# Performance work log

Hardware: AMD Instinct MI355X
Metric: run time of the kernel (lower is better)

Reference implementation:

```python
import jax, jax.numpy as jnp
import numpy as np

DIM, HEADS, DH, M, PINV_ITERS, RES_K = 512, 8, 64, 256, 6, 33

def layernorm(x, w, b, eps=1e-5):
    mu = jnp.mean(x, -1, keepdims=True)
    var = jnp.var(x, -1, keepdims=True)
    return (x - mu) * jax.lax.rsqrt(var + eps) * w + b

def pinv_iter(x, iters=PINV_ITERS):
    # Moore-Penrose iterative pseudo-inverse (lucidrains nystrom-attention)
    ax = jnp.abs(x)
    z = jnp.swapaxes(x, -1, -2) / (jnp.max(ax.sum(-1)) * jnp.max(ax.sum(-2)))
    I = jnp.eye(x.shape[-1], dtype=x.dtype)
    for _ in range(iters):
        xz = x @ z
        z = 0.25 * z @ (13 * I - xz @ (15 * I - xz @ (7 * I - xz)))
    return z

def _core(x, w_qkv):
    b, n, _ = x.shape
    pad = (M - n % M) % M            # Nystrom pads at the FRONT to a multiple of m=256
    xp = jnp.pad(x, ((0, 0), (pad, 0), (0, 0)))
    npad = n + pad
    q, k, v = jnp.split(xp @ w_qkv, 3, axis=-1)
    split_heads = lambda t: t.reshape(b, npad, HEADS, DH).transpose(0, 2, 1, 3)
    q = split_heads(q) * (DH ** -0.5)
    k, v = split_heads(k), split_heads(v)
    l = npad // M                    # tokens per landmark
    q_l = q.reshape(b, HEADS, M, l, DH).mean(3)
    k_l = k.reshape(b, HEADS, M, l, DH).mean(3)
    return q, k, v, q_l, k_l, pad, n

def nystrom_out(x, w_qkv, w_out, b_out, res_kernel):
    q, k, v, q_l, k_l, pad, n = _core(x, w_qkv)
    attn1 = jax.nn.softmax(jnp.einsum('bhid,bhjd->bhij', q, k_l), -1)    # (b,h,N,M)
    attn2 = jax.nn.softmax(jnp.einsum('bhid,bhjd->bhij', q_l, k_l), -1)  # (b,h,M,M)
    attn3 = jax.nn.softmax(jnp.einsum('bhid,bhjd->bhij', q_l, k), -1)    # (b,h,M,N)
    out = (attn1 @ pinv_iter(attn2)) @ (attn3 @ v)
    # depthwise residual conv over sequence dim, per head
    out = out + jax.lax.conv_general_dilated(
        v, res_kernel, (1, 1), [(RES_K // 2, RES_K // 2), (0, 0)],
        dimension_numbers=('NCHW', 'OIHW', 'NCHW'), feature_group_count=HEADS)
    b = out.shape[0]
    out = out.transpose(0, 2, 1, 3).reshape(b, -1, HEADS * DH) @ w_out + b_out
    return out[:, -n:]

def nystrom_cls_row(x, w_qkv):
    # cls-token (query index pad, head 0) row of attn1 @ pinv(attn2) @ attn3;
    # identical math to the full (n x n) matrix row the torch code slices out.
    q, k, v, q_l, k_l, pad, n = _core(x, w_qkv)
    q0, k0, ql0, kl0 = q[:, 0], k[:, 0], q_l[:, 0], k_l[:, 0]
    attn2 = jax.nn.softmax(ql0 @ jnp.swapaxes(kl0, -1, -2), -1)   # (b,M,M)
    attn3 = jax.nn.softmax(ql0 @ jnp.swapaxes(k0, -1, -2), -1)    # (b,M,N)
    row1 = jax.nn.softmax(jnp.einsum('bd,bjd->bj', q0[:, pad], kl0), -1)
    row = jnp.einsum('bj,bjk->bk', row1, pinv_iter(attn2))
    row = jnp.einsum('bk,bkn->bn', row, attn3)                    # (b, N_padded)
    return row, pad

def dwconv(x, k, b, p):
    y = jax.lax.conv_general_dilated(x, k, (1, 1), [(p, p), (p, p)],
        dimension_numbers=('NCHW', 'OIHW', 'NCHW'), feature_group_count=x.shape[1])
    return y + b[None, :, None, None]

def leff(x, k7, b7, k5, b5, k3, b3, Hs, Ws):
    cls_t, feat = x[:, :1], x[:, 1:]
    B, N, C = feat.shape
    img = feat.transpose(0, 2, 1).reshape(B, C, Hs, Ws)
    y = dwconv(img, k7, b7, 3) + img + dwconv(img, k5, b5, 2) + dwconv(img, k3, b3, 1)
    y = y.reshape(B, C, Hs * Ws).transpose(0, 2, 1)
    return jnp.concatenate([cls_t, y], axis=1)

def setup_inputs():
    key = jax.random.key(0)
    ks = iter(jax.random.split(key, 32))
    n, n_classes = 22500, 2
    p = {}
    p['h'] = jax.random.normal(next(ks), (n, 1024), jnp.float32)
    p['fc1_w'] = jax.random.normal(next(ks), (1024, DIM), jnp.float32) * 0.02
    p['fc1_b'] = jnp.zeros((DIM,), jnp.float32)
    p['cls_token'] = jax.random.normal(next(ks), (1, 1, DIM), jnp.float32)
    for pre in ('l1', 'l2'):
        p[pre + '_ln_w'] = jnp.ones((DIM,), jnp.float32)
        p[pre + '_ln_b'] = jnp.zeros((DIM,), jnp.float32)
        p[pre + '_wqkv'] = jax.random.normal(next(ks), (DIM, 3 * HEADS * DH), jnp.float32) * 0.02
        p[pre + '_wout'] = jax.random.normal(next(ks), (HEADS * DH, DIM), jnp.float32) * 0.02
        p[pre + '_bout'] = jnp.zeros((DIM,), jnp.float32)
        p[pre + '_resk'] = jax.random.normal(next(ks), (HEADS, 1, RES_K, 1), jnp.float32) * 0.05
    for kk in (7, 5, 3):
        p['leff_k%d' % kk] = jax.random.normal(next(ks), (DIM, 1, kk, kk), jnp.float32) * 0.05
        p['leff_b%d' % kk] = jnp.zeros((DIM,), jnp.float32)
    p['norm_w'] = jnp.ones((DIM,), jnp.float32)
    p['norm_b'] = jnp.zeros((DIM,), jnp.float32)
    p['fc2_w'] = jax.random.normal(next(ks), (DIM, n_classes), jnp.float32) * 0.02
    p['fc2_b'] = jnp.zeros((n_classes,), jnp.float32)
    return p

def reference(h, fc1_w, fc1_b, cls_token,
              l1_ln_w, l1_ln_b, l1_wqkv, l1_wout, l1_bout, l1_resk,
              leff_k7, leff_b7, leff_k5, leff_b5, leff_k3, leff_b3,
              l2_ln_w, l2_ln_b, l2_wqkv, l2_wout, l2_bout, l2_resk,
              norm_w, norm_b, fc2_w, fc2_b):
    x = h[None]                                   # (1, n, 1024)
    n = x.shape[1]
    x = jax.nn.relu(x @ fc1_w + fc1_b)            # (1, n, 512)
    Hs = int(np.ceil(np.sqrt(n)))                 # 150 for n=22500
    add_len = Hs * Hs - n
    if add_len > 0:
        x = jnp.concatenate([x, x[:, :add_len]], axis=1)
    x = jnp.concatenate([jnp.broadcast_to(cls_token, (1, 1, DIM)), x], axis=1)
    # TransLayer 1
    x = x + nystrom_out(layernorm(x, l1_ln_w, l1_ln_b), l1_wqkv, l1_wout, l1_bout, l1_resk)
    # LeFF positional layer
    x = leff(x, leff_k7, leff_b7, leff_k5, leff_b5, leff_k3, leff_b3, Hs, Hs)
    # TransLayer 2 (first call in TransMIL.forward)
    h2 = x + nystrom_out(layernorm(x, l2_ln_w, l2_ln_b), l2_wqkv, l2_wout, l2_bout, l2_resk)
    # TransLayer 2 second call: residual update then attention matrix of updated state
    h3 = h2 + nystrom_out(layernorm(h2, l2_ln_w, l2_ln_b), l2_wqkv, l2_wout, l2_bout, l2_resk)
    row, pad = nystrom_cls_row(layernorm(h3, l2_ln_w, l2_ln_b), l2_wqkv)
    A = row[0, pad + 1: pad + 1 + n][:, None]     # (n, 1) cls->instance attention
    hf = layernorm(h2, norm_w, norm_b)[:, 0]      # (1, 512)
    logits = hf @ fc2_w + fc2_b                   # (1, n_classes)
    Y_prob = jax.nn.softmax(logits, -1)
    return logits, Y_prob, A
```

## Files before the change

kernel.cpp:

```cpp
#include <hip/hip_runtime.h>

#define NTOK 22500
#define N1   22501
#define NPAD 22528
#define PADR 27
#define DIM  512
#define NH   8
#define DHD  64
#define MM   256
#define LLM  88
#define HSZ  150
#define CSZ  256
#define NCH  88

typedef short bf16x8 __attribute__((ext_vector_type(8)));
typedef float f32x4  __attribute__((ext_vector_type(4)));
typedef unsigned short us;

union U8 { bf16x8 v; unsigned short u[8]; };

__device__ __forceinline__ unsigned short f2b(float f){
  unsigned int u = __float_as_uint(f);
  unsigned int r = u + 0x7fffu + ((u>>16)&1u);
  return (unsigned short)(r>>16);
}
__device__ __forceinline__ float bf2f(unsigned short u){
  return __uint_as_float(((unsigned int)u)<<16);
}
__device__ __forceinline__ bf16x8 cvt8(float4 a, float4 b){
  U8 u;
  u.u[0]=f2b(a.x); u.u[1]=f2b(a.y); u.u[2]=f2b(a.z); u.u[3]=f2b(a.w);
  u.u[4]=f2b(b.x); u.u[5]=f2b(b.y); u.u[6]=f2b(b.z); u.u[7]=f2b(b.w);
  return u.v;
}
__device__ __forceinline__ void gld16(const void* g, void* l){
  __builtin_amdgcn_global_load_lds(
      (const __attribute__((address_space(1))) void*)g,
      (__attribute__((address_space(3))) void*)l, 16, 0, 0);
}

__device__ __forceinline__ float waveSum(float v){
#pragma unroll
  for (int o=32;o>0;o>>=1) v += __shfl_down(v,o);
  return v;
}
__device__ __forceinline__ float waveMax(float v){
#pragma unroll
  for (int o=32;o>0;o>>=1) v = fmaxf(v,__shfl_down(v,o));
  return v;
}
__device__ __forceinline__ float blockSum256(float v, float* sb){
  v = waveSum(v);
  __syncthreads();
  if ((threadIdx.x&63)==0) sb[threadIdx.x>>6]=v;
  __syncthreads();
  return sb[0]+sb[1]+sb[2]+sb[3];
}
__device__ __forceinline__ float blockMax256(float v, float* sb){
  v = waveMax(v);
  __syncthreads();
  if ((threadIdx.x&63)==0) sb[threadIdx.x>>6]=v;
  __syncthreads();
  return fmaxf(fmaxf(sb[0],sb[1]),fmaxf(sb[2],sb[3]));
}

__global__ void k_cvt(const float* __restrict__ src, us* __restrict__ dst, size_t n4)
{
  size_t i = ((size_t)blockIdx.x*256 + threadIdx.x);
  if (i < n4){
    float4 v = *(const float4*)(src + i*4);
    ushort4 u; u.x=f2b(v.x); u.y=f2b(v.y); u.z=f2b(v.z); u.w=f2b(v.w);
    *(ushort4*)(dst + i*4) = u;
  }
}

__global__ void k_wT(const float* __restrict__ W, us* __restrict__ Bt, int K, int N)
{
  __shared__ float tile[32][33];
  int tx = threadIdx.x&31, ty = threadIdx.x>>5;
  int k0 = blockIdx.x*32, n0 = blockIdx.y*32;
#pragma unroll
  for (int i=0;i<4;++i){
    int k = k0+ty+i*8;
    if (k<K && n0+tx<N) tile[ty+i*8][tx] = W[(size_t)k*N + n0+tx];
  }
  __syncthreads();
#pragma unroll
  for (int i=0;i<4;++i){
    int n = n0+ty+i*8, k = k0+tx;
    if (n<N && k<K) Bt[(size_t)n*K + k] = f2b(tile[tx][ty+i*8]);
  }
}

__global__ void k_vT(const us* __restrict__ V, us* __restrict__ Vt)
{
  __shared__ us tile[32][33];
  int tx = threadIdx.x&31, ty = threadIdx.x>>5;
  int p0 = blockIdx.x*32;
  int h = blockIdx.y>>1, d0 = (blockIdx.y&1)*32;
#pragma unroll
  for (int i=0;i<4;++i){
    int p = p0+ty+i*8;
    tile[ty+i*8][tx] = V[((size_t)h*NPAD+p)*DHD + d0+tx];
  }
  __syncthreads();
#pragma unroll
  for (int i=0;i<4;++i){
    int d = d0+ty+i*8;
    Vt[((size_t)h*DHD+d)*NPAD + p0+tx] = tile[tx][ty+i*8];
  }
}

template<int MODE>
__global__ __launch_bounds__(256) void k_gemm(
    const us* __restrict__ Ab, const us* __restrict__ Bt, const float* __restrict__ bias,
    us* __restrict__ Xb, float* __restrict__ Cf, float* __restrict__ C2,
    us* __restrict__ Q_, us* __restrict__ K_, us* __restrict__ V_,
    const us* __restrict__ zpg, int Kd, int mtn)
{
  constexpr int BM = 64;
  constexpr int BUFE = BM*64 + 128*64;
  __shared__ us SM[3*BUFE];
  const int tid = threadIdx.x;
  const int bid = blockIdx.x;
  const int ntile = bid / mtn;
  const int m0 = (bid % mtn)*BM, n0 = ntile*128;
  const int lane = tid & 63;
  const int wid = tid >> 6;
  const int wm = (wid>>1)*32, wn = (wid&1)*64;
  f32x4 acc[2][4] = {};
  const int NT = Kd >> 6;

  auto stage = [&](int t, int buf){
    us* As = SM + buf*BUFE;
    us* Bs = As + BM*64;
    int k0 = t*64;
#pragma unroll
    for (int i=0;i<2;++i){
      int c = wid*2+i;
      int row = c*8 + (lane>>3);
      int scol8 = ((lane&7) ^ (row&7))*8;
      int gm = m0+row;
      const us* ga;
      if (MODE==0)      ga = (gm<NTOK) ? Ab + (size_t)gm*Kd + k0 + scol8 : zpg + scol8;
      else if (MODE==2) ga = Ab + ((size_t)((gm<N1?gm:0)+PADR))*Kd + k0 + scol8;
      else              ga = (gm>=PADR) ? Ab + (size_t)(gm-PADR)*Kd + k0 + scol8 : zpg + scol8;
      gld16(ga, &As[c*512]);
    }
#pragma unroll
    for (int i=0;i<4;++i){
      int c = wid*4+i;
      int row = c*8 + (lane>>3);
      int scol8 = ((lane&7) ^ (row&7))*8;
      int vn = n0+row;
      if (MODE==3) vn = (vn<64)? vn : vn+448;
      gld16(Bt + (size_t)vn*Kd + k0 + scol8, &Bs[c*512]);
    }
  };

  stage(0, 0);
  stage(1, 1);
  for (int t=0; t<NT; ++t){
    asm volatile("s_waitcnt vmcnt(6)" ::: "memory");
    __builtin_amdgcn_s_barrier();
    asm volatile("" ::: "memory");
    if (t+2 < NT) stage(t+2, (t+2)%3);
    us* As = SM + (t%3)*BUFE;
    us* Bs = As + BM*64;
#pragma unroll
    for (int ks=0; ks<2; ++ks){
      const int kk = ks*32 + (lane>>4)*8;
      bf16x8 af[2], bfm[4];
#pragma unroll
      for (int tt=0;tt<2;++tt){
        int r = wm + tt*16 + (lane&15);
        af[tt] = *(bf16x8*)(&As[r*64 + (kk ^ ((r&7)<<3))]);
      }
#pragma unroll
      for (int tt=0;tt<4;++tt){
        int c = wn + tt*16 + (lane&15);
        bfm[tt] = *(bf16x8*)(&Bs[c*64 + (kk ^ ((c&7)<<3))]);
      }
#pragma unroll
      for (int mt=0;mt<2;++mt)
#pragma unroll
        for (int nt=0;nt<4;++nt)
          acc[mt][nt] = __builtin_amdgcn_mfma_f32_16x16x32_bf16(af[mt], bfm[nt], acc[mt][nt], 0,0,0);
    }
  }
  __syncthreads();
  const int rbase = (lane>>4)*4;
  const int cl = lane&15;
  if (MODE==3){
#pragma unroll
    for (int mt=0;mt<2;++mt)
#pragma unroll
      for (int r=0;r<4;++r){
        int gm = m0 + wm + mt*16 + rbase + r;
#pragma unroll
        for (int nt=0;nt<4;++nt){
          int gn = n0 + wn + nt*16 + cl;
          float v = acc[mt][nt][r];
          if (gn < 64) Cf[(size_t)gm*DHD + gn] = v*0.125f;
          else         C2[(size_t)gm*DHD + (gn-64)] = v;
        }
      }
    return;
  }
  const float sc1 = (MODE==1 && (ntile>>2)==0) ? 0.125f : 1.f;
#pragma unroll
  for (int mt=0;mt<2;++mt)
#pragma unroll
    for (int r=0;r<4;++r){
      int row = wm + mt*16 + rbase + r;
#pragma unroll
      for (int nt=0;nt<4;++nt){
        int col = wn + nt*16 + cl;
        float v = acc[mt][nt][r];
        if (MODE==0){ v += bias[n0+col]; v = v>0.f?v:0.f; }
        else if (MODE==2){ v += bias[n0+col]; }
        else v *= sc1;
        SM[row*128 + col] = f2b(v);
      }
    }
  __syncthreads();
  if (MODE==1){
    const int sec = ntile>>2;
    us* dst = sec==0 ? Q_ : (sec==1 ? K_ : V_);
#pragma unroll
    for (int i=0;i<4;++i){
      int v8 = i*256 + tid;
      int row = v8>>4, c8 = (v8&15)*8;
      int gm = m0 + row, gn = n0 + c8;
      int hh = (gn>>6)&7, d = gn&63;
      *(bf16x8*)(dst + ((size_t)hh*NPAD+gm)*DHD + d) = *(bf16x8*)(&SM[row*128 + c8]);
    }
  } else if (MODE==0){
#pragma unroll
    for (int i=0;i<4;++i){
      int v8 = i*256 + tid;
      int row = v8>>4, c8 = (v8&15)*8;
      int gm = m0 + row;
      if (gm < NTOK)
        *(bf16x8*)(Xb + (size_t)(1+gm)*DIM + n0 + c8) = *(bf16x8*)(&SM[row*128 + c8]);
    }
  } else {
#pragma unroll
    for (int i=0;i<4;++i){
      int v8 = i*256 + tid;
      int row = v8>>4, c8 = (v8&15)*8;
      int gm = m0 + row;
      if (gm < N1){
        us* p = Xb + (size_t)gm*DIM + n0 + c8;
        U8 xo, ad, o;
        xo.v = *(bf16x8*)p;
        ad.v = *(bf16x8*)(&SM[row*128 + c8]);
#pragma unroll
        for (int j=0;j<8;++j) o.u[j] = f2b(bf2f(xo.u[j]) + bf2f(ad.u[j]));
        *(bf16x8*)p = o.v;
      }
    }
  }
}

__global__ void k_setcls(us* __restrict__ X, const float* __restrict__ cls){
  int i = blockIdx.x*256 + threadIdx.x;
  if (i < DIM) X[i] = f2b(cls[i]);
}
__global__ void k_copyu(us* __restrict__ d, const us* __restrict__ s, size_t n){
  size_t i = (size_t)blockIdx.x*256 + threadIdx.x;
  if (i<n) d[i]=s[i];
}

__global__ void k_ln(const us* __restrict__ X, us* __restrict__ Y,
                     const float* __restrict__ w, const float* __restrict__ b)
{
  __shared__ float sb[4];
  const us* x = X + (size_t)blockIdx.x*DIM;
  us* y = Y + (size_t)blockIdx.x*DIM;
  int t = threadIdx.x;
  ushort2 xv = *(const ushort2*)(x + 2*t);
  float a0=bf2f(xv.x), a1=bf2f(xv.y);
  float s = blockSum256(a0+a1, sb);
  float q = blockSum256(a0*a0+a1*a1, sb);
  float mean = s*(1.f/512.f);
  float var = q*(1.f/512.f) - mean*mean;
  float rstd = rsqrtf(var+1e-5f);
  float2 wv = *(const float2*)(w + 2*t);
  float2 bv = *(const float2*)(b + 2*t);
  ushort2 o;
  o.x = f2b((a0-mean)*rstd*wv.x+bv.x);
  o.y = f2b((a1-mean)*rstd*wv.y+bv.y);
  *(ushort2*)(y + 2*t) = o;
}

__global__ void k_landmark2(const us* __restrict__ Q, const us* __restrict__ K,
                            us* __restrict__ QL, us* __restrict__ KL)
{
  int hm = blockIdx.x;
  bool isK = hm >= NH*MM;
  if (isK) hm -= NH*MM;
  int h = hm>>8, m = hm&255; int d = threadIdx.x;
  const us* base = (isK?K:Q) + ((size_t)h*NPAD + (size_t)m*LLM)*DHD + d;
  float s = 0.f;
  for (int j=0;j<LLM;++j) s += bf2f(base[(size_t)j*DHD]);
  (isK?KL:QL)[((size_t)h*MM + m)*DHD + d] = f2b(s * (1.f/(float)LLM));
}
__global__ void k_landmark2f(const float* __restrict__ Q, const float* __restrict__ K,
                             float* __restrict__ QL, float* __restrict__ KL)
{
  int hm = blockIdx.x;
  bool isK = hm >= MM;
  int m = isK ? hm-MM : hm; int d = threadIdx.x;
  const float* base = (isK?K:Q) + (size_t)m*LLM*DHD + d;
  float s = 0.f;
  for (int j=0;j<LLM;++j) s += base[(size_t)j*DHD];
  (isK?KL:QL)[(size_t)m*DHD + d] = s * (1.f/(float)LLM);
}

__global__ __launch_bounds__(64) void k_nt64(const float* __restrict__ A,
    const float* __restrict__ B, float* __restrict__ C,
    long sA, long sB, long sC, int Nr)
{
  int lane = threadIdx.x;
  int n0 = blockIdx.x*64, m0 = blockIdx.y*64;
  A += (size_t)blockIdx.z*sA; B += (size_t)blockIdx.z*sB; C += (size_t)blockIdx.z*sC;
  f32x4 acc[4][4] = {};
#pragma unroll
  for (int ks=0;ks<2;++ks){
    int kk = ks*32 + (lane>>4)*8;
    bf16x8 af[4], bfr[4];
#pragma unroll
    for (int mt=0;mt<4;++mt){
      const float* p = A + (size_t)(m0+mt*16+(lane&15))*64 + kk;
      af[mt] = cvt8(*(const float4*)p, *(const float4*)(p+4));
    }
#pragma unroll
    for (int nt=0;nt<4;++nt){
      const float* p = B + (size_t)(n0+nt*16+(lane&15))*64 + kk;
      bfr[nt] = cvt8(*(const float4*)p, *(const float4*)(p+4));
    }
#pragma unroll
    for (int mt=0;mt<4;++mt)
#pragma unroll
      for (int nt=0;nt<4;++nt)
        acc[mt][nt] = __builtin_amdgcn_mfma_f32_16x16x32_bf16(af[mt], bfr[nt], acc[mt][nt], 0,0,0);
  }
#pragma unroll
  for (int mt=0;mt<4;++mt)
#pragma unroll
    for (int r=0;r<4;++r){
      int row = m0+mt*16+(lane>>4)*4+r;
#pragma unroll
      for (int nt=0;nt<4;++nt){
        int col = n0+nt*16+(lane&15);
        C[(size_t)row*Nr + col] = acc[mt][nt][r];
      }
    }
}

__global__ __launch_bounds__(64) void k_nt64b(const us* __restrict__ A,
    const us* __restrict__ B, float* __restrict__ C,
    long sA, long sB, long sC, int Nr)
{
  int lane = threadIdx.x;
  int n0 = blockIdx.x*64, m0 = blockIdx.y*64;
  A += (size_t)blockIdx.z*sA; B += (size_t)blockIdx.z*sB; C += (size_t)blockIdx.z*sC;
  f32x4 acc[4][4] = {};
#pragma unroll
  for (int ks=0;ks<2;++ks){
    int kk = ks*32 + (lane>>4)*8;
    bf16x8 af[4], bfr[4];
#pragma unroll
    for (int mt=0;mt<4;++mt)
      af[mt] = *(const bf16x8*)(A + (size_t)(m0+mt*16+(lane&15))*64 + kk);
#pragma unroll
    for (int nt=0;nt<4;++nt)
      bfr[nt] = *(const bf16x8*)(B + (size_t)(n0+nt*16+(lane&15))*64 + kk);
#pragma unroll
    for (int mt=0;mt<4;++mt)
#pragma unroll
      for (int nt=0;nt<4;++nt)
        acc[mt][nt] = __builtin_amdgcn_mfma_f32_16x16x32_bf16(af[mt], bfr[nt], acc[mt][nt], 0,0,0);
  }
#pragma unroll
  for (int mt=0;mt<4;++mt)
#pragma unroll
    for (int r=0;r<4;++r){
      int row = m0+mt*16+(lane>>4)*4+r;
#pragma unroll
      for (int nt=0;nt<4;++nt){
        int col = n0+nt*16+(lane&15);
        C[(size_t)row*Nr + col] = acc[mt][nt][r];
      }
    }
}

template<int PM>
__global__ __launch_bounds__(256) void k_pgemm(const us* __restrict__ A,
    const us* __restrict__ Bt, us* __restrict__ C, us* __restrict__ Ct,
    float dc, float alpha, int writeC)
{
  __shared__ us As[64*256];
  __shared__ us Bs[64*256];
  const int tid = threadIdx.x, lane = tid&63, wid = tid>>6;
  const int n0 = blockIdx.x*64, m0 = blockIdx.y*64;
  const us* Ab = A + (size_t)blockIdx.z*65536;
  const us* Bb = Bt + (size_t)blockIdx.z*65536;
  for (int i=tid; i<4096; i+=256){
    int r = i>>6, c4 = (i&63)*4;
    *(ushort4*)(&As[r*256 + (c4 ^ ((r&7)<<3))]) = *(const ushort4*)(Ab + (size_t)(m0+r)*256 + c4);
    *(ushort4*)(&Bs[r*256 + (c4 ^ ((r&7)<<3))]) = *(const ushort4*)(Bb + (size_t)(n0+r)*256 + c4);
  }
  __syncthreads();
  const int wm = (wid>>1)*32, wn = (wid&1)*32;
  f32x4 acc[2][2] = {};
#pragma unroll
  for (int ks=0;ks<8;++ks){
    int kk = ks*32 + (lane>>4)*8;
    bf16x8 af[2], bfr[2];
#pragma unroll
    for (int t=0;t<2;++t){
      int rr = wm + t*16 + (lane&15);
      af[t] = *(const bf16x8*)(&As[rr*256 + (kk ^ ((rr&7)<<3))]);
      int cc = wn + t*16 + (lane&15);
      bfr[t] = *(const bf16x8*)(&Bs[cc*256 + (kk ^ ((cc&7)<<3))]);
    }
#pragma unroll
    for (int mt=0;mt<2;++mt)
#pragma unroll
      for (int nt=0;nt<2;++nt)
        acc[mt][nt] = __builtin_amdgcn_mfma_f32_16x16x32_bf16(af[mt], bfr[nt], acc[mt][nt], 0,0,0);
  }
  float vv[2][4][2];
#pragma unroll
  for (int mt=0;mt<2;++mt)
#pragma unroll
    for (int q=0;q<4;++q){
      int rl = wm + mt*16 + (lane>>4)*4 + q;
#pragma unroll
      for (int nt=0;nt<2;++nt){
        int clx = wn + nt*16 + (lane&15);
        float v = acc[mt][nt][q];
        if (PM==1) v = alpha*(dc*bf2f(As[rl*256 + (clx ^ ((rl&7)<<3))]) - v);
        vv[mt][q][nt] = v;
      }
    }
  __syncthreads();
  us* TT = As;
#pragma unroll
  for (int mt=0;mt<2;++mt)
#pragma unroll
    for (int q=0;q<4;++q){
      int rl = wm + mt*16 + (lane>>4)*4 + q;
      int sw = (rl&7)<<3;
#pragma unroll
      for (int nt=0;nt<2;++nt){
        int clx = wn + nt*16 + (lane&15);
        TT[rl*64 + (clx ^ sw)] = f2b(vv[mt][q][nt]);
      }
    }
  __syncthreads();
  {
    int c = tid>>2, r0 = (tid&3)*16;
    U8 b0, b1;
#pragma unroll
    for (int i=0;i<8;++i){
      int r = r0+i;       b0.u[i] = TT[r*64 + (c ^ ((r&7)<<3))];
      int r2 = r0+8+i;    b1.u[i] = TT[r2*64 + (c ^ ((r2&7)<<3))];
    }
    us* dst = Ct + (size_t)blockIdx.z*65536 + (size_t)(n0+c)*256 + m0 + r0;
    *(bf16x8*)dst = b0.v;
    *(bf16x8*)(dst+8) = b1.v;
  }
  if (PM==0 || writeC){
    int rr = tid>>2, c0 = (tid&3)*16;
    int sw = (rr&7)<<3;
    bf16x8 x0 = *(const bf16x8*)(&TT[rr*64 + (c0 ^ sw)]);
    bf16x8 x1 = *(const bf16x8*)(&TT[rr*64 + ((c0+8) ^ sw)]);
    us* dc2 = C + (size_t)blockIdx.z*65536 + (size_t)(m0+rr)*256 + n0 + c0;
    *(bf16x8*)dc2 = x0;
    *(bf16x8*)(dc2+8) = x1;
  }
}

__global__ __launch_bounds__(256) void k_pgemm2(const us* __restrict__ A,
    const us* __restrict__ Bt, us* __restrict__ Ct)
{
  __shared__ us As[16384];
  __shared__ us Bs[16384];
  const int tid = threadIdx.x, lane = tid&63, wid = tid>>6;
  const int n0 = 0, m0 = blockIdx.y*64;
  const us* Ab = A + (size_t)blockIdx.z*65536;
  const us* Bb = Bt + (size_t)blockIdx.z*16384;
  for (int i=tid; i<4096; i+=256){
    int r = i>>6, c4 = (i&63)*4;
    *(ushort4*)(&As[r*256 + (c4 ^ ((r&7)<<3))]) = *(const ushort4*)(Ab + (size_t)(m0+r)*256 + c4);
    if (r < 64)
      *(ushort4*)(&Bs[r*256 + (c4 ^ ((r&7)<<3))]) = *(const ushort4*)(Bb + (size_t)(n0+r)*256 + c4);
  }
  __syncthreads();
  const int wm = (wid>>1)*32, wn = (wid&1)*32;
  f32x4 acc[2][2] = {};
#pragma unroll
  for (int ks=0;ks<8;++ks){
    int kk = ks*32 + (lane>>4)*8;
    bf16x8 af[2], bfr[2];
#pragma unroll
    for (int t=0;t<2;++t){
      int rr = wm + t*16 + (lane&15);
      af[t] = *(const bf16x8*)(&As[rr*256 + (kk ^ ((rr&7)<<3))]);
      int cc = wn + t*16 + (lane&15);
      bfr[t] = *(const bf16x8*)(&Bs[cc*256 + (kk ^ ((cc&7)<<3))]);
    }
#pragma unroll
    for (int mt=0;mt<2;++mt)
#pragma unroll
      for (int nt=0;nt<2;++nt)
        acc[mt][nt] = __builtin_amdgcn_mfma_f32_16x16x32_bf16(af[mt], bfr[nt], acc[mt][nt], 0,0,0);
  }
#pragma unroll
  for (int mt=0;mt<2;++mt)
#pragma unroll
    for (int r=0;r<4;++r){
      int row = m0 + wm + mt*16 + (lane>>4)*4 + r;
#pragma unroll
      for (int nt=0;nt<2;++nt){
        int col = n0 + wn + nt*16 + (lane&15);
        Ct[(size_t)blockIdx.z*16384 + (size_t)col*256 + row] = f2b(acc[mt][nt][r]);
      }
    }
}

__global__ void k_softmax256(float* __restrict__ S, us* __restrict__ Sb)
{
  __shared__ float sb[4];
  float* row = S + ((size_t)blockIdx.x<<8);
  float x = row[threadIdx.x];
  float m = blockMax256(x, sb);
  float e = __expf(x-m);
  float s = blockSum256(e, sb);
  float p = e/s;
  row[threadIdx.x] = p;
  Sb[((size_t)blockIdx.x<<8) + threadIdx.x] = f2b(p);
}
__global__ void k_csmax(const float* __restrict__ A2, float* __restrict__ sums)
{
  __shared__ float sb[4];
  int b = blockIdx.x, j = threadIdx.x;
  const float* Ab = A2 + ((size_t)b<<16);
  float s = 0.f;
  for (int i=0;i<256;++i) s += Ab[((size_t)i<<8)+j];
  float m = blockMax256(s, sb);
  if (j==0) sums[b] = m;
}
__global__ void k_scale2(const float* __restrict__ sums, float* __restrict__ scl, int nb)
{
  __shared__ float sb[4];
  float m=-1e30f;
  for (int i=threadIdx.x;i<nb;i+=256) m = fmaxf(m, sums[i]);
  m = blockMax256(m, sb);
  if (threadIdx.x==0) scl[0] = 1.f/m;
}
__global__ void k_z0t(const float* __restrict__ A2, us* __restrict__ Z, us* __restrict__ Zt,
                      const float* __restrict__ scl)
{
  __shared__ us tile[32][33];
  int tx = threadIdx.x&31, ty = threadIdx.x>>5;
  int i0 = blockIdx.x*32;
  int head = blockIdx.y>>3, j0 = (blockIdx.y&7)*32;
  float s = scl[0];
  const float* Ab = A2 + (size_t)head*65536;
  us* Zh  = Z  + (size_t)head*65536;
  us* Zth = Zt + (size_t)head*65536;
#pragma unroll
  for (int ii=0;ii<4;++ii){
    int i = i0+ty+ii*8;
    us bv = f2b(Ab[(size_t)i*256 + j0+tx]*s);
    Zth[(size_t)i*256 + j0+tx] = bv;
    tile[ty+ii*8][tx] = bv;
  }
  __syncthreads();
#pragma unroll
  for (int ii=0;ii<4;++ii){
    int j = j0+ty+ii*8;
    Zh[(size_t)j*256 + i0+tx] = tile[tx][ty+ii*8];
  }
}

__global__ __launch_bounds__(512) void k_attn3(const us* __restrict__ QLb,
    const us* __restrict__ Kb, const us* __restrict__ Vt,
    float* __restrict__ Pmax, float* __restrict__ Psum, us* __restrict__ Pacc)
{
  __shared__ us Ks[64*64];
  __shared__ us Vs[64*64];
  __shared__ us Ps[8*32*64];
  int h = blockIdx.y, cx = blockIdx.x;
  int tid = threadIdx.x, wid = tid>>6, lane = tid&63;
  bf16x8 aq[2][2];
#pragma unroll
  for (int mt=0;mt<2;++mt){
    const us* qp = QLb + ((size_t)h*MM + wid*32 + mt*16 + (lane&15))*DHD;
#pragma unroll
    for (int ks=0;ks<2;++ks)
      aq[mt][ks] = *(const bf16x8*)(qp + ks*32 + (lane>>4)*8);
  }
  float m_[2][4], l_[2][4];
  f32x4 acc[2][4] = {};
#pragma unroll
  for (int mt=0;mt<2;++mt)
#pragma unroll
    for (int r=0;r<4;++r){ m_[mt][r] = -1e30f; l_[mt][r] = 0.f; }

  us* Pw = &Ps[wid*2048];
  for (int t=0;t<4;++t){
    int kb0 = cx*CSZ + t*64;
    __syncthreads();
    for (int i=tid;i<1024;i+=512){
      int rr = i>>4, c4 = (i&15)*4;
      ushort4 ku = *(const ushort4*)(Kb + ((size_t)h*NPAD + kb0 + rr)*DHD + c4);
      *(ushort4*)(&Ks[rr*64 + (c4 ^ ((rr&7)<<3))]) = ku;
      ushort4 vu = *(const ushort4*)(Vt + ((size_t)h*DHD + rr)*NPAD + kb0 + c4);
      *(ushort4*)(&Vs[rr*64 + (c4 ^ ((rr&7)<<3))]) = vu;
    }
    __syncthreads();
    f32x4 s[2][4] = {};
    __builtin_amdgcn_s_setprio(1);
#pragma unroll
    for (int ks=0;ks<2;++ks){
      int kk = ks*32 + (lane>>4)*8;
      bf16x8 kbf[4];
#pragma unroll
      for (int nt=0;nt<4;++nt){
        int key = nt*16 + (lane&15);
        kbf[nt] = *(const bf16x8*)(&Ks[key*64 + (kk ^ ((key&7)<<3))]);
      }
#pragma unroll
      for (int mt=0;mt<2;++mt)
#pragma unroll
        for (int nt=0;nt<4;++nt)
          s[mt][nt] = __builtin_amdgcn_mfma_f32_16x16x32_bf16(aq[mt][ks], kbf[nt], s[mt][nt], 0,0,0);
    }
    __builtin_amdgcn_s_setprio(0);
#pragma unroll
    for (int mt=0;mt<2;++mt){
#pragma unroll
      for (int r=0;r<4;++r){
        float mx = fmaxf(fmaxf(s[mt][0][r], s[mt][1][r]), fmaxf(s[mt][2][r], s[mt][3][r]));
#pragma unroll
        for (int off=8;off>=1;off>>=1) mx = fmaxf(mx, __shfl_xor(mx, off));
        float mn = fmaxf(m_[mt][r], mx);
        float f = __expf(m_[mt][r]-mn);
        float la = 0.f;
#pragma unroll
        for (int nt=0;nt<4;++nt){ float p=__expf(s[mt][nt][r]-mn); s[mt][nt][r]=p; la+=p; }
#pragma unroll
        for (int off=8;off>=1;off>>=1) la += __shfl_xor(la, off);
        l_[mt][r] = l_[mt][r]*f + la;
        m_[mt][r] = mn;
#pragma unroll
        for (int dt=0;dt<4;++dt) acc[mt][dt][r] *= f;
      }
    }
#pragma unroll
    for (int mt=0;mt<2;++mt)
#pragma unroll
      for (int r=0;r<4;++r){
        int row = mt*16 + (lane>>4)*4 + r;
        int sw = (row&7)<<3;
#pragma unroll
        for (int nt=0;nt<4;++nt){
          int col = nt*16 + (lane&15);
          Pw[row*64 + (col ^ sw)] = f2b(s[mt][nt][r]);
        }
      }
    __builtin_amdgcn_s_setprio(1);
#pragma unroll
    for (int ks=0;ks<2;++ks){
      int kk = ks*32 + (lane>>4)*8;
      bf16x8 pa[2], vb[4];
#pragma unroll
      for (int mt=0;mt<2;++mt){
        int arow = mt*16 + (lane&15);
        pa[mt] = *(const bf16x8*)(&Pw[arow*64 + (kk ^ ((arow&7)<<3))]);
      }
#pragma unroll
      for (int dt=0;dt<4;++dt){
        int d = dt*16 + (lane&15);
        vb[dt] = *(const bf16x8*)(&Vs[d*64 + (kk ^ ((d&7)<<3))]);
      }
#pragma unroll
      for (int mt=0;mt<2;++mt)
#pragma unroll
        for (int dt=0;dt<4;++dt)
          acc[mt][dt] = __builtin_amdgcn_mfma_f32_16x16x32_bf16(pa[mt], vb[dt], acc[mt][dt], 0,0,0);
    }
    __builtin_amdgcn_s_setprio(0);
  }
  size_t pbase = ((size_t)h*NCH + cx)*MM;
#pragma unroll
  for (int mt=0;mt<2;++mt)
#pragma unroll
    for (int r=0;r<4;++r){
      int row = wid*32 + mt*16 + (lane>>4)*4 + r;
      if ((lane&15)==0){ Pmax[pbase+row]=m_[mt][r]; Psum[pbase+row]=l_[mt][r]; }
#pragma unroll
      for (int dt=0;dt<4;++dt)
        Pacc[(pbase+row)*DHD + dt*16+(lane&15)] = f2b(acc[mt][dt][r]);
    }
}

__global__ void k_attn3_merge(const float* __restrict__ Pmax, const float* __restrict__ Psum,
    const us* __restrict__ Pacc, us* __restrict__ A3Vtb)
{
  int hm = blockIdx.x; int h = hm>>8, m = hm&255; int d = threadIdx.x;
  float gm = -1e30f;
  for (int c=0;c<NCH;++c) gm = fmaxf(gm, Pmax[((size_t)h*NCH+c)*MM+m]);
  float tot=0.f, acc=0.f;
  for (int c=0;c<NCH;++c){
    size_t pi = ((size_t)h*NCH+c)*MM+m;
    float w = __expf(Pmax[pi]-gm);
    tot += Psum[pi]*w;
    acc += bf2f(Pacc[pi*DHD+d])*w;
  }
  A3Vtb[((size_t)h*DHD + d)*MM + m] = f2b(acc/tot);
}

__global__ __launch_bounds__(256) void k_attn1(const us* __restrict__ Qb,
    const us* __restrict__ KLb, const us* __restrict__ WmT,
    us* __restrict__ OH)
{
  __shared__ us KWs[64*256];
  __shared__ us Ps[64*256];
  int h = blockIdx.y, tid = threadIdx.x;
  int wid = tid>>6, lane = tid&63;
  int q0 = blockIdx.x*64;
  for (int i=tid; i<4096; i+=256){
    int lm = i>>4, k4 = (i&15)*4;
    *(ushort4*)(&KWs[lm*64 + (k4 ^ ((lm&7)<<3))]) =
        *(const ushort4*)(KLb + ((size_t)h*MM + lm)*DHD + k4);
  }
  bf16x8 aq[2];
  const us* qp = Qb + ((size_t)h*NPAD + q0 + wid*16 + (lane&15))*DHD;
#pragma unroll
  for (int ks=0;ks<2;++ks)
    aq[ks] = *(const bf16x8*)(qp + ks*32 + (lane>>4)*8);
  __syncthreads();
  f32x4 s[16];
#pragma unroll
  for (int nt=0;nt<16;++nt) s[nt] = (f32x4){0.f,0.f,0.f,0.f};
  __builtin_amdgcn_s_setprio(1);
#pragma unroll
  for (int ks=0;ks<2;++ks){
    int kk = ks*32 + (lane>>4)*8;
#pragma unroll
    for (int nt=0;nt<16;++nt){
      int col = nt*16 + (lane&15);
      bf16x8 b = *(const bf16x8*)(&KWs[col*64 + (kk ^ ((col&7)<<3))]);
      s[nt] = __builtin_amdgcn_mfma_f32_16x16x32_bf16(aq[ks], b, s[nt], 0,0,0);
    }
  }
  __builtin_amdgcn_s_setprio(0);
  float rcp[4];
#pragma unroll
  for (int r=0;r<4;++r){
    float m = -1e30f;
#pragma unroll
    for (int nt=0;nt<16;++nt) m = fmaxf(m, s[nt][r]);
#pragma unroll
    for (int off=8;off>=1;off>>=1) m = fmaxf(m, __shfl_xor(m, off));
    float l = 0.f;
#pragma unroll
    for (int nt=0;nt<16;++nt){ float p=__expf(s[nt][r]-m); s[nt][r]=p; l+=p; }
#pragma unroll
    for (int off=8;off>=1;off>>=1) l += __shfl_xor(l, off);
    rcp[r] = 1.f/l;
  }
  int prow_base = wid*16 + (lane>>4)*4;
#pragma unroll
  for (int nt=0;nt<16;++nt){
    int col = nt*16 + (lane&15);
#pragma unroll
    for (int r=0;r<4;++r){
      int row = prow_base + r;
      Ps[row*256 + (col ^ ((row&7)<<3))] = f2b(s[nt][r]);
    }
  }
  __syncthreads();
  for (int i=tid; i<4096; i+=256){
    int d = i>>6, k4 = (i&63)*4;
    ushort4 u = *(const ushort4*)(WmT + ((size_t)h*DHD + d)*MM + k4);
    *(ushort4*)(&KWs[d*256 + (k4 ^ ((d&7)<<3))]) = u;
  }
  __syncthreads();
  f32x4 acc[4] = {};
  int arow = wid*16 + (lane&15);
  __builtin_amdgcn_s_setprio(1);
#pragma unroll
  for (int ks=0;ks<8;++ks){
    int kk = ks*32 + (lane>>4)*8;
    bf16x8 a = *(const bf16x8*)(&Ps[arow*256 + (kk ^ ((arow&7)<<3))]);
#pragma unroll
    for (int dt=0;dt<4;++dt){
      int d = dt*16 + (lane&15);
      bf16x8 b = *(const bf16x8*)(&KWs[d*256 + (kk ^ ((d&7)<<3))]);
      acc[dt] = __builtin_amdgcn_mfma_f32_16x16x32_bf16(a, b, acc[dt], 0,0,0);
    }
  }
  __builtin_amdgcn_s_setprio(0);
#pragma unroll
  for (int r=0;r<4;++r){
    int row = q0 + prow_base + r;
    us* op = OH + (size_t)row*DIM + h*DHD;
#pragma unroll
    for (int dt=0;dt<4;++dt)
      op[dt*16 + (lane&15)] = f2b(acc[dt][r]*rcp[r]);
  }
}

#define SCBLK 32
__global__ __launch_bounds__(256) void k_seqconv(const us* __restrict__ Vb,
    const float* __restrict__ resk, us* __restrict__ OH)
{
  __shared__ us Vs[64*512];
  int tid = threadIdx.x;
  int p0 = blockIdx.x*SCBLK;
  for (int i=tid; i<16384; i+=256){
    int pl = i>>8, c2 = i&255;
    int gp = p0 - 16 + pl;
    int hh = c2>>5, d2 = (c2&31)*2;
    ushort2 v = make_ushort2(0,0);
    if (gp>=0 && gp<NPAD) v = *(const ushort2*)(Vb + ((size_t)hh*NPAD+gp)*DHD + d2);
    *(ushort2*)(&Vs[pl*512 + c2*2]) = v;
  }
  __syncthreads();
  int h = tid>>5;
  float kr[33];
#pragma unroll
  for (int r=0;r<33;++r) kr[r] = resk[h*33+r];
  for (int pl=0; pl<SCBLK; ++pl){
    float s0=0.f, s1=0.f;
#pragma unroll
    for (int r=0;r<33;++r){
      ushort2 v = *(const ushort2*)(&Vs[(pl+r)*512 + tid*2]);
      s0 += bf2f(v.x)*kr[r];
      s1 += bf2f(v.y)*kr[r];
    }
    size_t o = (size_t)(p0+pl)*DIM + tid*2;
    ushort2 cur = *(ushort2*)(OH + o);
    *(ushort2*)(OH + o) = make_ushort2(f2b(bf2f(cur.x)+s0), f2b(bf2f(cur.y)+s1));
  }
}

__global__ void k_tfwd(const us* __restrict__ X, us* __restrict__ T)
{
  __shared__ us tile[32][33];
  int tx = threadIdx.x & 31, ty = threadIdx.x >> 5;
  int s0 = blockIdx.x*32, c0 = blockIdx.y*32;
  for (int yy=0; yy<4; ++yy){
    int s = s0 + ty + yy*8;
    if (s < NTOK) tile[ty+yy*8][tx] = X[(size_t)(1+s)*DIM + c0+tx];
  }
  __syncthreads();
  for (int yy=0; yy<4; ++yy){
    int c = c0 + ty + yy*8;
    int s = s0 + tx;
    if (s < NTOK) T[(size_t)c*NTOK + s] = tile[tx][ty+yy*8];
  }
}
__global__ void k_tbwd(const us* __restrict__ T, us* __restrict__ X)
{
  __shared__ us tile[32][33];
  int tx = threadIdx.x & 31, ty = threadIdx.x >> 5;
  int s0 = blockIdx.x*32, c0 = blockIdx.y*32;
  for (int yy=0; yy<4; ++yy){
    int c = c0 + ty + yy*8, s = s0 + tx;
    if (s < NTOK) tile[ty+yy*8][tx] = T[(size_t)c*NTOK + s];
  }
  __syncthreads();
  for (int yy=0; yy<4; ++yy){
    int s = s0 + ty + yy*8, c = c0 + tx;
    if (s < NTOK) X[(size_t)(1+s)*DIM + c] = tile[tx][ty+yy*8];
  }
}
__global__ __launch_bounds__(256) void k_leff(const us* __restrict__ T,
    const float* __restrict__ k7, const float* __restrict__ b7,
    const float* __restrict__ k5, const float* __restrict__ b5,
    const float* __restrict__ k3, const float* __restrict__ b3,
    us* __restrict__ T2)
{
  __shared__ float tile[21*21];
  int c = blockIdx.y;
  int ti = blockIdx.x/10, tj = blockIdx.x%10;
  int i0 = ti*15-3, j0 = tj*15-3;
  const us* img = T + (size_t)c*NTOK;
  for (int idx=threadIdx.x; idx<441; idx+=256){
    int ii = idx/21, jj = idx%21;
    int gi = i0+ii, gj = j0+jj;
    tile[idx] = (gi>=0 && gi<HSZ && gj>=0 && gj<HSZ) ? bf2f(img[gi*HSZ+gj]) : 0.f;
  }
  __syncthreads();
  if (threadIdx.x < 225){
    int li = threadIdx.x/15, lj = threadIdx.x%15;
    int gi = ti*15+li, gj = tj*15+lj;
    float acc = tile[(li+3)*21 + (lj+3)] + b7[c]+b5[c]+b3[c];
    const float* w7 = k7 + c*49;
#pragma unroll
    for (int a=0;a<7;++a)
#pragma unroll
      for (int bb=0;bb<7;++bb) acc += tile[(li+a)*21 + (lj+bb)]*w7[a*7+bb];
    const float* w5 = k5 + c*25;
#pragma unroll
    for (int a=0;a<5;++a)
#pragma unroll
      for (int bb=0;bb<5;++bb) acc += tile[(li+1+a)*21 + (lj+1+bb)]*w5[a*5+bb];
    const float* w3 = k3 + c*9;
#pragma unroll
    for (int a=0;a<3;++a)
#pragma unroll
      for (int bb=0;bb<3;++bb) acc += tile[(li+2+a)*21 + (lj+2+bb)]*w3[a*3+bb];
    T2[(size_t)c*NTOK + gi*HSZ+gj] = f2b(acc);
  }
}

__global__ void k_row1(const float* __restrict__ Q0, const float* __restrict__ KL0,
                       float* __restrict__ row1)
{
  __shared__ float sb[4];
  __shared__ float qv[64];
  int t = threadIdx.x;
  if (t<64) qv[t] = Q0[PADR*DHD + t];
  __syncthreads();
  float l = 0.f;
#pragma unroll
  for (int d=0;d<64;++d) l += qv[d]*KL0[(size_t)t*DHD+d];
  float m = blockMax256(l, sb);
  float e = __expf(l-m);
  float s = blockSum256(e, sb);
  row1[t] = e/s;
}
__global__ void k_rz(const float* __restrict__ row1, const us* __restrict__ Zt,
                     float* __restrict__ rz)
{
  __shared__ float r1[256];
  int t = threadIdx.x;
  r1[t] = row1[t];
  __syncthreads();
  float s = 0.f;
  for (int k2=0;k2<256;++k2) s += r1[k2]*bf2f(Zt[(size_t)t*MM + k2]);
  rz[t] = s;
}
__global__ void k_rowstat(const float* __restrict__ L0, float* __restrict__ mx, float* __restrict__ se)
{
  __shared__ float sb[4];
  const float* row = L0 + (size_t)blockIdx.x*NPAD;
  float m = -1e30f;
  for (int i=threadIdx.x;i<NPAD;i+=256) m = fmaxf(m, row[i]);
  m = blockMax256(m, sb);
  float s = 0.f;
  for (int i=threadIdx.x;i<NPAD;i+=256) s += __expf(row[i]-m);
  s = blockSum256(s, sb);
  if (threadIdx.x==0){ mx[blockIdx.x]=m; se[blockIdx.x]=s; }
}
__global__ void k_aout(const float* __restrict__ L0, const float* __restrict__ rz,
    const float* __restrict__ mx, const float* __restrict__ se, float* __restrict__ out)
{
  __shared__ float wk[256], mk[256];
  int t = threadIdx.x;
  wk[t] = rz[t]/se[t];
  mk[t] = mx[t];
  __syncthreads();
  int p = blockIdx.x*256 + t;
  if (p >= NTOK) return;
  size_t pp = (size_t)(PADR+1+p);
  float a = 0.f;
  for (int k2=0;k2<256;++k2) a += wk[k2]*__expf(L0[(size_t)k2*NPAD+pp]-mk[k2]);
  out[4+p] = a;
}
__global__ void k_final(const us* __restrict__ H2r, const float* __restrict__ nw,
    const float* __restrict__ nbb, const float* __restrict__ w2, const float* __restrict__ b2,
    float* __restrict__ out)
{
  __shared__ float sb[4];
  __shared__ float hf[512];
  int t = threadIdx.x;
  float x0 = bf2f(H2r[t]), x1 = bf2f(H2r[256+t]);
  float s = blockSum256(x0+x1, sb);
  float q = blockSum256(x0*x0+x1*x1, sb);
  float mean = s*(1.f/512.f);
  float var = q*(1.f/512.f) - mean*mean;
  float rstd = rsqrtf(var+1e-5f);
  hf[t]     = (x0-mean)*rstd*nw[t]+nbb[t];
  hf[256+t] = (x1-mean)*rstd*nw[256+t]+nbb[256+t];
  __syncthreads();
  float p0 = hf[t]*w2[t*2]   + hf[256+t]*w2[(256+t)*2];
  float p1 = hf[t]*w2[t*2+1] + hf[256+t]*w2[(256+t)*2+1];
  p0 = blockSum256(p0, sb);
  p1 = blockSum256(p1, sb);
  if (t==0){
    float l0 = p0+b2[0], l1 = p1+b2[1];
    float m = fmaxf(l0,l1);
    float e0 = __expf(l0-m), e1 = __expf(l1-m), si = 1.f/(e0+e1);
    out[0]=l0; out[1]=l1; out[2]=e0*si; out[3]=e1*si;
  }
}

struct Bufs {
  float *A2,*sums,*scl,*Pmax,*Psum;
  us *Xb,*Yb,*OHb,*Qb,*Kb,*Vb,*Vtb,*QLb,*KLb,*A2b;
  us *Z0b,*Z0tb,*Z1b,*Z1tb,*XZb,*XZtb,*T1tb,*T2tb;
  us *A3Vtb,*WmT,*Pacc,*zpg;
};

static void run_pinv(const us* A2b, Bufs& b, int NB, hipStream_t st)
{
  dim3 g(4,4,NB);
  us *Zc=b.Z0b, *Zct=b.Z0tb, *Zn=b.Z1b, *Znt=b.Z1tb;
  for (int it=0; it<6; ++it){
    k_pgemm<0><<<g,256,0,st>>>(A2b, Zct, b.XZb, b.XZtb, 0.f, 1.f, 1);
    k_pgemm<1><<<g,256,0,st>>>(b.XZb, b.XZtb, nullptr, b.T1tb, 7.f, 1.f, 0);
    k_pgemm<1><<<g,256,0,st>>>(b.XZb, b.T1tb, nullptr, b.T2tb, 15.f, 1.f, 0);
    k_pgemm<1><<<g,256,0,st>>>(Zc, b.T2tb, Zn, Znt, 13.f, 0.25f, 1);
    us* t1=Zc; Zc=Zn; Zn=t1;
    us* t2=Zct; Zct=Znt; Znt=t2;
  }
}

static void nystrom_layer(Bufs& b, const float* lnw, const float* lnb,
    const us* wqkvT, const us* woutT,
    const float* bout, const float* resk, hipStream_t st)
{
  k_ln<<<N1,256,0,st>>>(b.Xb, b.Yb, lnw, lnb);
  k_gemm<1><<<352*12,256,0,st>>>(b.Yb, wqkvT, nullptr,
      nullptr, nullptr, nullptr, b.Qb, b.Kb, b.Vb, b.zpg, DIM, 352);
  k_vT<<<dim3(NPAD/32,16),256,0,st>>>(b.Vb, b.Vtb);
  k_landmark2<<<2*NH*MM,64,0,st>>>(b.Qb, b.Kb, b.QLb, b.KLb);
  k_nt64b<<<dim3(4,4,NH),64,0,st>>>(b.QLb, b.KLb, b.A2,
      (long)MM*DHD,(long)MM*DHD,(long)MM*MM, MM);
  k_softmax256<<<NH*MM,256,0,st>>>(b.A2, b.A2b);
  k_csmax<<<NH,256,0,st>>>(b.A2, b.sums);
  k_scale2<<<1,256,0,st>>>(b.sums, b.scl, NH);
  k_z0t<<<dim3(8,8*NH),256,0,st>>>(b.A2, b.Z0b, b.Z0tb, b.scl);
  run_pinv(b.A2b, b, NH, st);
  k_attn3<<<dim3(NCH,NH),512,0,st>>>(b.QLb, b.Kb, b.Vtb, b.Pmax, b.Psum, b.Pacc);
  k_attn3_merge<<<NH*MM,64,0,st>>>(b.Pmax, b.Psum, b.Pacc, b.A3Vtb);
  k_pgemm2<<<dim3(1,4,NH),256,0,st>>>(b.Z0b, b.A3Vtb, b.WmT);
  k_attn1<<<dim3(NPAD/64,NH),256,0,st>>>(b.Qb, b.KLb, b.WmT, b.OHb);
  k_seqconv<<<NPAD/SCBLK,256,0,st>>>(b.Vb, resk, b.OHb);
  k_gemm<2><<<352*4,256,0,st>>>(b.OHb, woutT, bout,
      b.Xb, nullptr, nullptr, nullptr, nullptr, nullptr, b.zpg, DIM, 352);
}

extern "C" void kernel_launch(void* const* d_in, const int* in_sizes, int n_in,
                              void* d_out, int out_size, void* d_ws, size_t ws_size,
                              hipStream_t stream)
{
  (void)n_in; (void)out_size;
  bool sig_order = (in_sizes[10] == 25088);
  int iL2 = sig_order ? 16 : 10;
  int iLf = sig_order ? 10 : 16;

  const float* h       = (const float*)d_in[0];
  const float* fc1_w   = (const float*)d_in[1];
  const float* fc1_b   = (const float*)d_in[2];
  const float* cls_tok = (const float*)d_in[3];
  const float* l1_lnw  = (const float*)d_in[4];
  const float* l1_lnb  = (const float*)d_in[5];
  const float* l1_wqkv = (const float*)d_in[6];
  const float* l1_wout = (const float*)d_in[7];
  const float* l1_bout = (const float*)d_in[8];
  const float* l1_resk = (const float*)d_in[9];
  const float* l2_lnw  = (const float*)d_in[iL2+0];
  const float* l2_lnb  = (const float*)d_in[iL2+1];
  const float* l2_wqkv = (const float*)d_in[iL2+2];
  const float* l2_wout = (const float*)d_in[iL2+3];
  const float* l2_bout = (const float*)d_in[iL2+4];
  const float* l2_resk = (const float*)d_in[iL2+5];
  const float* k7 = (const float*)d_in[iLf+0];
  const float* b7 = (const float*)d_in[iLf+1];
  const float* k5 = (const float*)d_in[iLf+2];
  const float* b5 = (const float*)d_in[iLf+3];
  const float* k3 = (const float*)d_in[iLf+4];
  const float* b3 = (const float*)d_in[iLf+5];
  const float* nw = (const float*)d_in[22];
  const float* nbb= (const float*)d_in[23];
  const float* w2 = (const float*)d_in[24];
  const float* b2 = (const float*)d_in[25];
  float* out = (float*)d_out;

  char* base = (char*)d_ws;
  auto allocF = [&](size_t n)->float*{
    float* p=(float*)base; base += ((n*sizeof(float)+255)&~(size_t)255); return p; };
  auto allocU = [&](size_t n)->us*{
    us* p=(us*)base; base += ((n*sizeof(us)+255)&~(size_t)255); return p; };

  const size_t S = (size_t)NPAD*DIM;
  const size_t SQ = (size_t)MM*MM;
  Bufs b;
  b.Xb  = allocU(S);
  b.Yb  = allocU(S);
  b.OHb = allocU(S);
  b.Qb  = allocU(S);
  b.Kb  = allocU(S);
  b.Vb  = allocU(S);
  b.Vtb = allocU(S);
  b.QLb = allocU((size_t)NH*MM*DHD);
  b.KLb = allocU((size_t)NH*MM*DHD);
  b.A2  = allocF((size_t)NH*SQ);
  b.A2b = allocU((size_t)NH*SQ);
  b.Z0b = allocU((size_t)NH*SQ);  b.Z0tb = allocU((size_t)NH*SQ);
  b.Z1b = allocU((size_t)NH*SQ);  b.Z1tb = allocU((size_t)NH*SQ);
  b.XZb = allocU((size_t)NH*SQ);  b.XZtb = allocU((size_t)NH*SQ);
  b.T1tb= allocU((size_t)NH*SQ);
  b.T2tb= allocU((size_t)NH*SQ);
  b.A3Vtb = allocU((size_t)NH*MM*DHD);
  b.WmT   = allocU((size_t)NH*MM*DHD);
  b.sums  = allocF(2*(size_t)NH*MM);
  b.scl   = allocF(16);
  b.Pmax  = allocF((size_t)NH*NCH*MM);
  b.Psum  = allocF((size_t)NH*NCH*MM);
  b.Pacc  = allocU((size_t)NH*NCH*MM*DHD);
  b.zpg   = allocU(512);
  us* hb     = allocU((size_t)NTOK*1024);
  us* fc1T   = allocU((size_t)DIM*1024);
  us* wqkvT1 = allocU((size_t)1536*DIM);
  us* wqkvT2 = allocU((size_t)1536*DIM);
  us* woutT1 = allocU((size_t)DIM*DIM);
  us* woutT2 = allocU((size_t)DIM*DIM);
  float* Q0   = allocF((size_t)NPAD*DHD);
  float* K0   = allocF((size_t)NPAD*DHD);
  float* QL0f = allocF((size_t)MM*DHD);
  float* KL0f = allocF((size_t)MM*DHD);
  float* row1 = allocF(256);
  float* rzv  = allocF(256);
  float* mxv  = allocF(256);
  float* sev  = allocF(256);
  us* h2row = allocU(512);
  if ((size_t)(base - (char*)d_ws) > ws_size) return;

  hipMemsetAsync((void*)b.zpg, 0, 1024, stream);

  k_cvt<<<((size_t)NTOK*1024/4 + 255)/256,256,0,stream>>>(h, hb, (size_t)NTOK*1024/4);
  k_wT<<<dim3(32,16),256,0,stream>>>(fc1_w, fc1T, 1024, DIM);
  k_wT<<<dim3(16,48),256,0,stream>>>(l1_wqkv, wqkvT1, DIM, 1536);
  k_wT<<<dim3(16,48),256,0,stream>>>(l2_wqkv, wqkvT2, DIM, 1536);
  k_wT<<<dim3(16,16),256,0,stream>>>(l1_wout, woutT1, DIM, DIM);
  k_wT<<<dim3(16,16),256,0,stream>>>(l2_wout, woutT2, DIM, DIM);

  k_gemm<0><<<352*4,256,0,stream>>>(hb, fc1T, fc1_b,
      b.Xb, nullptr, nullptr, nullptr, nullptr, nullptr, b.zpg, 1024, 352);
  k_setcls<<<2,256,0,stream>>>(b.Xb, cls_tok);

  nystrom_layer(b, l1_lnw, l1_lnb, wqkvT1, woutT1, l1_bout, l1_resk, stream);
  k_tfwd<<<dim3(704,16),256,0,stream>>>(b.Xb, b.OHb);
  k_leff<<<dim3(100,512),256,0,stream>>>(b.OHb, k7,b7,k5,b5,k3,b3, b.Qb);
  k_tbwd<<<dim3(704,16),256,0,stream>>>(b.Qb, b.Xb);

  nystrom_layer(b, l2_lnw, l2_lnb, wqkvT2, woutT2, l2_bout, l2_resk, stream);
  k_copyu<<<2,256,0,stream>>>(h2row, b.Xb, 512);

  nystrom_layer(b, l2_lnw, l2_lnb, wqkvT2, woutT2, l2_bout, l2_resk, stream);

  k_ln<<<N1,256,0,stream>>>(b.Xb, b.Yb, l2_lnw, l2_lnb);
  k_gemm<3><<<352,256,0,stream>>>(b.Yb, wqkvT2, nullptr,
      nullptr, Q0, K0, nullptr, nullptr, nullptr, b.zpg, DIM, 352);
  k_landmark2f<<<2*MM,64,0,stream>>>(Q0, K0, QL0f, KL0f);
  k_nt64<<<dim3(4,4,1),64,0,stream>>>(QL0f, KL0f, b.A2, 0,0,0, MM);
  k_softmax256<<<MM,256,0,stream>>>(b.A2, b.A2b);
  k_csmax<<<1,256,0,stream>>>(b.A2, b.sums);
  k_scale2<<<1,256,0,stream>>>(b.sums, b.scl, 1);
  k_z0t<<<dim3(8,8),256,0,stream>>>(b.A2, b.Z0b, b.Z0tb, b.scl);
  run_pinv(b.A2b, b, 1, stream);
  k_row1<<<1,256,0,stream>>>(Q0, KL0f, row1);
  k_rz<<<1,256,0,stream>>>(row1, b.Z0tb, rzv);
  float* L0 = (float*)b.Yb;
  k_nt64<<<dim3(NPAD/64,4,1),64,0,stream>>>(QL0f, K0, L0, 0,0,0, NPAD);
  k_rowstat<<<MM,256,0,stream>>>(L0, mxv, sev);
  k_aout<<<88,256,0,stream>>>(L0, rzv, mxv, sev, out);
  k_final<<<1,256,0,stream>>>(h2row, nw, nbb, w2, b2, out);
}
```

Measured before the change: 2.247 ms.

## Retile LeFF depthwise conv to 64x15 tiles with register column reuse

```diff
diff --git a/kernel.cpp b/kernel.cpp
--- a/kernel.cpp
+++ b/kernel.cpp
@@ -889,37 +889,65 @@
     const float* __restrict__ k3, const float* __restrict__ b3,
     us* __restrict__ T2)
 {
-  __shared__ float tile[21*21];
-  int c = blockIdx.y;
-  int ti = blockIdx.x/10, tj = blockIdx.x%10;
-  int i0 = ti*15-3, j0 = tj*15-3;
+  __shared__ float tile[70*22];
+  __shared__ float wbuf[84];
+  const int c = blockIdx.y;
+  const int ti = blockIdx.x/10, tj = blockIdx.x%10;
+  const int gbase = ti*64, col0 = tj*15;
+  const int t = threadIdx.x;
+  if (t < 49) wbuf[t] = k7[c*49+t];
+  else if (t < 74) wbuf[t] = k5[c*25 + t-49];
+  else if (t < 83) wbuf[t] = k3[c*9 + t-74];
+  else if (t == 83) wbuf[83] = b7[c]+b5[c]+b3[c];
   const us* img = T + (size_t)c*NTOK;
-  for (int idx=threadIdx.x; idx<441; idx+=256){
-    int ii = idx/21, jj = idx%21;
-    int gi = i0+ii, gj = j0+jj;
-    tile[idx] = (gi>=0 && gi<HSZ && gj>=0 && gj<HSZ) ? bf2f(img[gi*HSZ+gj]) : 0.f;
-  }
-  __syncthreads();
-  if (threadIdx.x < 225){
-    int li = threadIdx.x/15, lj = threadIdx.x%15;
-    int gi = ti*15+li, gj = tj*15+lj;
-    float acc = tile[(li+3)*21 + (lj+3)] + b7[c]+b5[c]+b3[c];
-    const float* w7 = k7 + c*49;
-#pragma unroll
-    for (int a=0;a<7;++a)
-#pragma unroll
-      for (int bb=0;bb<7;++bb) acc += tile[(li+a)*21 + (lj+bb)]*w7[a*7+bb];
-    const float* w5 = k5 + c*25;
-#pragma unroll
-    for (int a=0;a<5;++a)
-#pragma unroll
-      for (int bb=0;bb<5;++bb) acc += tile[(li+1+a)*21 + (lj+1+bb)]*w5[a*5+bb];
-    const float* w3 = k3 + c*9;
-#pragma unroll
-    for (int a=0;a<3;++a)
-#pragma unroll
-      for (int bb=0;bb<3;++bb) acc += tile[(li+2+a)*21 + (lj+2+bb)]*w3[a*3+bb];
-    T2[(size_t)c*NTOK + gi*HSZ+gj] = f2b(acc);
+  for (int idx=t; idx<1470; idx+=256){
+    int r = idx/21, cc = idx%21;
+    int gi = gbase-3+r, gj = col0-3+cc;
+    tile[r*22+cc] = (gi>=0 && gi<HSZ && gj>=0 && gj<HSZ) ? bf2f(img[gi*HSZ+gj]) : 0.f;
+  }
+  __syncthreads();
+  if (t >= 240) return;
+  const int lj = t%15, rg = t/15;
+  const int R0 = rg*4;
+  float o[4];
+#pragma unroll
+  for (int k=0;k<4;++k) o[k] = wbuf[83];
+#pragma unroll
+  for (int bb=0; bb<7; ++bb){
+    float col[10];
+#pragma unroll
+    for (int i=0;i<10;++i) col[i] = tile[(R0+i)*22 + lj+bb];
+#pragma unroll
+    for (int a=0;a<7;++a){
+      float w = wbuf[a*7+bb];
+#pragma unroll
+      for (int k=0;k<4;++k) o[k] += w*col[k+a];
+    }
+    if (bb>=1 && bb<=5){
+#pragma unroll
+      for (int a=0;a<5;++a){
+        float w = wbuf[49 + a*5 + (bb-1)];
+#pragma unroll
+        for (int k=0;k<4;++k) o[k] += w*col[k+1+a];
+      }
+    }
+    if (bb>=2 && bb<=4){
+#pragma unroll
+      for (int a=0;a<3;++a){
+        float w = wbuf[74 + a*3 + (bb-2)];
+#pragma unroll
+        for (int k=0;k<4;++k) o[k] += w*col[k+2+a];
+      }
+    }
+    if (bb==3){
+#pragma unroll
+      for (int k=0;k<4;++k) o[k] += col[k+3];
+    }
+  }
+#pragma unroll
+  for (int k=0;k<4;++k){
+    int gi = gbase + R0 + k;
+    if (gi < HSZ) T2[(size_t)c*NTOK + gi*HSZ + col0+lj] = f2b(o[k]);
   }
 }
 
@@ -1153,7 +1181,7 @@
 
   nystrom_layer(b, l1_lnw, l1_lnb, wqkvT1, woutT1, l1_bout, l1_resk, stream);
   k_tfwd<<<dim3(704,16),256,0,stream>>>(b.Xb, b.OHb);
-  k_leff<<<dim3(100,512),256,0,stream>>>(b.OHb, k7,b7,k5,b5,k3,b3, b.Qb);
+  k_leff<<<dim3(30,512),256,0,stream>>>(b.OHb, k7,b7,k5,b5,k3,b3, b.Qb);
   k_tbwd<<<dim3(704,16),256,0,stream>>>(b.Qb, b.Xb);
 
   nystrom_layer(b, l2_lnw, l2_lnb, wqkvT2, woutT2, l2_bout, l2_resk, stream);
```

Result: no change. 2.262 ms (+0.7%).

## Fuse pinv iteration GEMMs into one cooperative kernel with grid syncs

Applied to the files above, without the earlier changes.

```diff
diff --git a/kernel.cpp b/kernel.cpp
--- a/kernel.cpp
+++ b/kernel.cpp
@@ -1,4 +1,5 @@
 #include <hip/hip_runtime.h>
+#include <hip/hip_cooperative_groups.h>
 
 #define NTOK 22500
 #define N1   22501
@@ -397,12 +398,10 @@
 }
 
 template<int PM>
-__global__ __launch_bounds__(256) void k_pgemm(const us* __restrict__ A,
+__device__ __forceinline__ void pgemm_tile(const us* __restrict__ A,
     const us* __restrict__ Bt, us* __restrict__ C, us* __restrict__ Ct,
-    float dc, float alpha, int writeC)
-{
-  __shared__ us As[64*256];
-  __shared__ us Bs[64*256];
+    float dc, float alpha, int writeC, us* As, us* Bs)
+{
   const int tid = threadIdx.x, lane = tid&63, wid = tid>>6;
   const int n0 = blockIdx.x*64, m0 = blockIdx.y*64;
   const us* Ab = A + (size_t)blockIdx.z*65536;
@@ -481,6 +480,28 @@
     us* dc2 = C + (size_t)blockIdx.z*65536 + (size_t)(m0+rr)*256 + n0 + c0;
     *(bf16x8*)dc2 = x0;
     *(bf16x8*)(dc2+8) = x1;
+  }
+}
+
+__global__ __launch_bounds__(256) void k_pinv(const us* __restrict__ A2b,
+    us* Z0, us* Z0t, us* Z1, us* Z1t,
+    us* XZ, us* XZt, us* T1t, us* T2t)
+{
+  __shared__ us As[64*256];
+  __shared__ us Bs[64*256];
+  cooperative_groups::grid_group grid = cooperative_groups::this_grid();
+  us *Zc=Z0, *Zct=Z0t, *Zn=Z1, *Znt=Z1t;
+  for (int it=0; it<6; ++it){
+    pgemm_tile<0>(A2b, Zct, XZ, XZt, 0.f, 1.f, 1, As, Bs);
+    grid.sync();
+    pgemm_tile<1>(XZ, XZt, nullptr, T1t, 7.f, 1.f, 0, As, Bs);
+    grid.sync();
+    pgemm_tile<1>(XZ, T1t, nullptr, T2t, 15.f, 1.f, 0, As, Bs);
+    grid.sync();
+    pgemm_tile<1>(Zc, T2t, Zn, Znt, 13.f, 0.25f, 1, As, Bs);
+    grid.sync();
+    us* s1=Zc; Zc=Zn; Zn=s1;
+    us* s2=Zct; Zct=Znt; Znt=s2;
   }
 }
 
@@ -1014,16 +1035,12 @@
 
 static void run_pinv(const us* A2b, Bufs& b, int NB, hipStream_t st)
 {
-  dim3 g(4,4,NB);
-  us *Zc=b.Z0b, *Zct=b.Z0tb, *Zn=b.Z1b, *Znt=b.Z1tb;
-  for (int it=0; it<6; ++it){
-    k_pgemm<0><<<g,256,0,st>>>(A2b, Zct, b.XZb, b.XZtb, 0.f, 1.f, 1);
-    k_pgemm<1><<<g,256,0,st>>>(b.XZb, b.XZtb, nullptr, b.T1tb, 7.f, 1.f, 0);
-    k_pgemm<1><<<g,256,0,st>>>(b.XZb, b.T1tb, nullptr, b.T2tb, 15.f, 1.f, 0);
-    k_pgemm<1><<<g,256,0,st>>>(Zc, b.T2tb, Zn, Znt, 13.f, 0.25f, 1);
-    us* t1=Zc; Zc=Zn; Zn=t1;
-    us* t2=Zct; Zct=Znt; Znt=t2;
-  }
+  dim3 g(4,4,NB), blk(256,1,1);
+  const us* a = A2b;
+  us *z0=b.Z0b, *z0t=b.Z0tb, *z1=b.Z1b, *z1t=b.Z1tb;
+  us *xz=b.XZb, *xzt=b.XZtb, *t1=b.T1tb, *t2=b.T2tb;
+  void* args[] = {&a,&z0,&z0t,&z1,&z1t,&xz,&xzt,&t1,&t2};
+  hipLaunchCooperativeKernel((void*)k_pinv, g, blk, args, 0, st);
 }
 
 static void nystrom_layer(Bufs& b, const float* lnw, const float* lnb,
```

Measured after the change: 3.479 ms. 1.55x slower.
